# Optimization experiments

Measured on AMD Instinct MI355X. Metric: run time of the kernel, lower is better.

The kernel has to match this reference:

```python
import jax, jax.numpy as jnp
import numpy as np

H_HEADS = 8
EPS = 1e-5

def layernorm(x, g, b):
    m = jnp.mean(x, axis=-1, keepdims=True)
    v = jnp.mean(jnp.square(x - m), axis=-1, keepdims=True)
    return (x - m) * jax.lax.rsqrt(v + EPS) * g + b

def setup_inputs() -> dict:
    key = jax.random.key(0)
    ks = jax.random.split(key, 8)
    B, H, W, C = 8, 64, 64, 256
    C2 = 2 * C
    s = lambda n: 1.0 / np.sqrt(n)
    return {
        "x1": jax.random.normal(ks[0], (B, H, W, C), jnp.float32),
        "x2": jax.random.normal(ks[1], (B, H, W, C), jnp.float32),
        "norm1_g": jnp.ones((C,)), "norm1_b": jnp.zeros((C,)),
        "lin_w": jax.random.normal(ks[2], (C, C), jnp.float32) * s(C),
        "lin_b": jnp.zeros((C,)),
        "reproj_w": jax.random.normal(ks[3], (C, C), jnp.float32) * s(C),
        "reproj_b": jnp.zeros((C,)),
        "attn_norm_g": jnp.ones((C,)), "attn_norm_b": jnp.zeros((C,)),
        "norm2_g": jnp.ones((C,)), "norm2_b": jnp.zeros((C,)),
        "fc1_w": jax.random.normal(ks[4], (C2, C), jnp.float32) * s(C),
        "fc1_b": jnp.zeros((C2,)),
        "dw_w": jax.random.normal(ks[5], (C2, 1, 3, 3), jnp.float32) * s(9),
        "dw_b": jnp.zeros((C2,)),
        "ffn_n1_g": jnp.ones((C2,)), "ffn_n1_b": jnp.zeros((C2,)),
        "fc2_w": jax.random.normal(ks[6], (C, C2), jnp.float32) * s(C2),
        "fc2_b": jnp.zeros((C,)),
        "ffn_n3_g": jnp.ones((C,)), "ffn_n3_b": jnp.zeros((C,)),
    }

def reference(x1, x2, norm1_g, norm1_b, lin_w, lin_b, reproj_w, reproj_b,
              attn_norm_g, attn_norm_b, norm2_g, norm2_b, fc1_w, fc1_b,
              dw_w, dw_b, ffn_n1_g, ffn_n1_b, fc2_w, fc2_b, ffn_n3_g, ffn_n3_b):
    B, H, W, C = x1.shape
    N = H * W
    h = H_HEADS
    dk = C // h  # head key channels; value_dim == key_dim == C here
    # shared norm1 + linear projection of both streams
    n1 = layernorm(x1, norm1_g, norm1_b) @ lin_w.T + lin_b  # (B,H,W,C) queries src
    n2 = layernorm(x2, norm1_g, norm1_b) @ lin_w.T + lin_b  # (B,H,W,C) key/value src
    # (B,N,C) -> (B,h,d,N); channel dim split contiguously per head (matches torch slicing)
    q = jnp.transpose(n1.reshape(B, N, h, dk), (0, 2, 3, 1))
    k = jnp.transpose(n2.reshape(B, N, h, dk), (0, 2, 3, 1))
    v = k  # values are the same tensor slices (value_dim == key_dim)
    k = jax.nn.softmax(k, axis=-1)   # softmax over tokens N
    q = jax.nn.softmax(q, axis=2)    # softmax over head channel dim
    # linear attention: context (B,h,dk,dv), then project back to tokens
    context = jnp.einsum('bhdn,bhvn->bhdv', k, v)
    att = jnp.einsum('bhdv,bhdn->bhvn', context, q)  # (B,h,dv,N)
    agg = att.reshape(B, C, H, W)
    # 1x1 conv reprojection (value_channels -> key_channels)
    rep = jnp.einsum('bvhw,kv->bhwk', agg, reproj_w) + reproj_b  # (B,H,W,C)
    attn_out = layernorm(rep, attn_norm_g, attn_norm_b)
    # out_proj is Identity since key_dim == in_dim
    tx = attn_out + x1
    y = layernorm(tx, norm2_g, norm2_b)  # skip_ffn input
    # skip_ffn
    h1 = y @ fc1_w.T + fc1_b  # (B,H,W,2C)
    hc = jnp.transpose(h1, (0, 3, 1, 2))  # NCHW
    dw = jax.lax.conv_general_dilated(
        hc, dw_w, window_strides=(1, 1), padding='SAME',
        dimension_numbers=('NCHW', 'OIHW', 'NCHW'),
        feature_group_count=hc.shape[1])
    dw = jnp.transpose(dw + dw_b[None, :, None, None], (0, 2, 3, 1))  # NHWC
    ax = jax.nn.gelu(layernorm(dw, ffn_n1_g, ffn_n1_b), approximate=False)
    out = ax @ fc2_w.T + fc2_b
    return layernorm(out + y, ffn_n3_g, ffn_n3_b)
```

## Files before the change

### kernel.cpp

```cpp
#include <hip/hip_runtime.h>

#define BTOK 32768
#define CC 256
#define CC2 512
#define NBATCH 8

typedef __bf16 bf16x8 __attribute__((ext_vector_type(8)));
typedef float f32x4 __attribute__((ext_vector_type(4)));
typedef unsigned short u16x8 __attribute__((ext_vector_type(8)));
typedef unsigned short u16x4 __attribute__((ext_vector_type(4)));

__device__ __forceinline__ float b2f(unsigned short u) {
    return __uint_as_float(((unsigned)u) << 16);
}
__device__ __forceinline__ unsigned short f2b(float f) {
    unsigned x = __float_as_uint(f);
    return (unsigned short)((x + 0x7fffu + ((x >> 16) & 1u)) >> 16);
}
__device__ __forceinline__ float wredsum(float v) {
#pragma unroll
    for (int m = 1; m < 64; m <<= 1) v += __shfl_xor(v, m);
    return v;
}
__device__ __forceinline__ float grp4sum(float v) {
    v += __shfl_xor(v, 1);
    v += __shfl_xor(v, 2);
    return v;
}

typedef __attribute__((address_space(3))) unsigned int lds_u32;
typedef const __attribute__((address_space(1))) unsigned int glb_u32;
__device__ __forceinline__ void gload_lds16(const unsigned short* g, unsigned short* l) {
    __builtin_amdgcn_global_load_lds((glb_u32*)g, (lds_u32*)l, 16, 0, 0);
}

__global__ __launch_bounds__(256) void probe_kernel(
    const unsigned short* __restrict__ x, int* __restrict__ flag)
{
    int t = threadIdx.x;
    int c = 0;
    for (int i = t; i < 1024; i += 256) {
        unsigned e = (x[i] >> 7) & 0xFFu;
        c += (e >= 110u && e <= 135u) ? 1 : 0;
    }
#pragma unroll
    for (int m = 1; m < 64; m <<= 1) c += __shfl_xor(c, m);
    __shared__ int acc[4];
    if ((t & 63) == 0) acc[t >> 6] = c;
    __syncthreads();
    if (t == 0) *flag = ((acc[0] + acc[1] + acc[2] + acc[3]) >= 896) ? 1 : 0;
}

__global__ __launch_bounds__(256) void cvt_params_kernel(
    const int* __restrict__ flagp,
    const void* p0, const void* p1, const void* p2, const void* p3, const void* p4,
    const void* p5, const void* p6, const void* p7, const void* p8, const void* p9,
    const void* p10, const void* p11, const void* p12, const void* p13, const void* p14,
    const void* p15, const void* p16, const void* p17, const void* p18, const void* p19,
    unsigned short* __restrict__ dst)
{
    bool isb = (*flagp != 0);
    long g = (long)blockIdx.x * 256 + threadIdx.x;
    long str = (long)gridDim.x * 256;
#define CVT(src, off, n)                                                        \
    for (long i = g; i < (long)(n); i += str)                                   \
        dst[(off) + i] = isb ? ((const unsigned short*)(src))[i]                \
                             : f2b(((const float*)(src))[i]);
    CVT(p0, 0, 256)
    CVT(p1, 256, 256)
    CVT(p2, 512, 65536)
    CVT(p3, 66048, 256)
    CVT(p4, 66304, 65536)
    CVT(p5, 131840, 256)
    CVT(p6, 132096, 256)
    CVT(p7, 132352, 256)
    CVT(p8, 132608, 256)
    CVT(p9, 132864, 256)
    CVT(p10, 133120, 131072)
    CVT(p11, 264192, 512)
    for (long i = g; i < 4608; i += str) {
        int tap = (int)(i >> 9), c = (int)(i & 511);
        dst[264704 + i] = isb ? ((const unsigned short*)p12)[c * 9 + tap]
                              : f2b(((const float*)p12)[c * 9 + tap]);
    }
    CVT(p13, 269312, 512)
    CVT(p14, 269824, 512)
    CVT(p15, 270336, 512)
    CVT(p16, 270848, 131072)
    CVT(p17, 401920, 256)
    CVT(p18, 402176, 256)
    CVT(p19, 402432, 256)
#undef CVT
}

__global__ __launch_bounds__(256) void ln_dual_kernel(
    const void* __restrict__ x1, const void* __restrict__ x2,
    const unsigned short* __restrict__ g, const unsigned short* __restrict__ b,
    unsigned short* __restrict__ out, const int* __restrict__ flagp)
{
    bool isb = (*flagp != 0);
    int wid = threadIdx.x >> 6, l = threadIdx.x & 63;
    long row = (long)blockIdx.x * 4 + wid;
    const void* xsel = (row < BTOK) ? x1 : x2;
    long r = (row < BTOK) ? row : (row - BTOK);
    float f[4];
    if (isb) {
        u16x4 v = *reinterpret_cast<const u16x4*>((const unsigned short*)xsel + r * CC + l * 4);
#pragma unroll
        for (int j = 0; j < 4; j++) f[j] = b2f(v[j]);
    } else {
        f32x4 v = *reinterpret_cast<const f32x4*>((const float*)xsel + r * CC + l * 4);
#pragma unroll
        for (int j = 0; j < 4; j++) f[j] = v[j];
    }
    float mean = wredsum(f[0] + f[1] + f[2] + f[3]) * (1.f / CC);
    float d[4], sq = 0.f;
#pragma unroll
    for (int j = 0; j < 4; j++) { d[j] = f[j] - mean; sq += d[j] * d[j]; }
    float rs = rsqrtf(wredsum(sq) * (1.f / CC) + 1e-5f);
    u16x4 gv = *reinterpret_cast<const u16x4*>(g + l * 4);
    u16x4 bv = *reinterpret_cast<const u16x4*>(b + l * 4);
    u16x4 o;
#pragma unroll
    for (int j = 0; j < 4; j++) o[j] = f2b(d[j] * rs * b2f(gv[j]) + b2f(bv[j]));
    *reinterpret_cast<u16x4*>(out + row * CC + l * 4) = o;
}

template<int K>
__global__ __launch_bounds__(256) void gemm_lds_kernel(
    const unsigned short* __restrict__ A, const unsigned short* __restrict__ Wt,
    const unsigned short* __restrict__ bias, unsigned short* __restrict__ out,
    int O, int nwg)
{
    __shared__ unsigned short Asm[3][4096];
    __shared__ unsigned short Bsm[3][4096];
    int t = threadIdx.x, l = t & 63, w = t >> 6;
    int bid = blockIdx.x, cpx = nwg >> 3;
    int wg = (bid & 7) * cpx + (bid >> 3);
    int ntn = O >> 7;
    long tm = (long)(wg / ntn) << 7;
    int tn = (wg % ntn) << 7;
    int wr = (w >> 1) << 6, wc = (w & 1) << 6;

    int rloc = t >> 2;
    int q = (t & 3) ^ ((t >> 3) & 3);
    const unsigned short* ga0 = A + (tm + rloc) * K + q * 8;
    const unsigned short* ga1 = ga0 + (long)64 * K;
    const unsigned short* gb0 = Wt + (long)(tn + rloc) * K + q * 8;
    const unsigned short* gb1 = gb0 + (long)64 * K;

    int rr = l & 15;
    int sA = ((l >> 4) ^ ((rr >> 1) & 3)) << 3;
    int aoff[4], boff[4];
#pragma unroll
    for (int m = 0; m < 4; m++) aoff[m] = (wr + m * 16 + rr) * 32 + sA;
#pragma unroll
    for (int n = 0; n < 4; n++) boff[n] = (wc + n * 16 + rr) * 32 + sA;

    f32x4 acc[4][4];
#pragma unroll
    for (int m = 0; m < 4; m++)
#pragma unroll
        for (int n = 0; n < 4; n++) acc[m][n] = {0.f, 0.f, 0.f, 0.f};

    auto stage = [&](int buf, int koff) {
        gload_lds16(ga0 + koff, &Asm[buf][w * 512]);
        gload_lds16(ga1 + koff, &Asm[buf][2048 + w * 512]);
        gload_lds16(gb0 + koff, &Bsm[buf][w * 512]);
        gload_lds16(gb1 + koff, &Bsm[buf][2048 + w * 512]);
    };
    auto compute = [&](int buf) {
        bf16x8 af[4], bfr[4];
#pragma unroll
        for (int m = 0; m < 4; m++) af[m] = *reinterpret_cast<const bf16x8*>(&Asm[buf][aoff[m]]);
#pragma unroll
        for (int n = 0; n < 4; n++) bfr[n] = *reinterpret_cast<const bf16x8*>(&Bsm[buf][boff[n]]);
#pragma unroll
        for (int m = 0; m < 4; m++)
#pragma unroll
            for (int n = 0; n < 4; n++)
                acc[m][n] = __builtin_amdgcn_mfma_f32_16x16x32_bf16(af[m], bfr[n], acc[m][n], 0, 0, 0);
    };

    constexpr int NK = K / 32;
    stage(0, 0);
    stage(1, 32);
    asm volatile("s_waitcnt vmcnt(4)" ::: "memory");
    __builtin_amdgcn_s_barrier();
    asm volatile("" ::: "memory");
#pragma unroll
    for (int kt = 0; kt < NK; kt++) {
        if (kt + 2 < NK) stage((kt + 2) % 3, (kt + 2) * 32);
        compute(kt % 3);
        if (kt + 1 < NK) {
            if (kt + 2 < NK) asm volatile("s_waitcnt vmcnt(4)" ::: "memory");
            else             asm volatile("s_waitcnt vmcnt(0)" ::: "memory");
            __builtin_amdgcn_s_barrier();
            asm volatile("" ::: "memory");
        }
    }

    int orow = (l >> 4) << 2;
    int ocol = l & 15;
    float bi[4];
#pragma unroll
    for (int n = 0; n < 4; n++) bi[n] = b2f(bias[tn + wc + n * 16 + ocol]);
#pragma unroll
    for (int m = 0; m < 4; m++) {
#pragma unroll
        for (int n = 0; n < 4; n++) {
#pragma unroll
            for (int j = 0; j < 4; j++) {
                out[(tm + wr + m * 16 + orow + j) * O + tn + wc + n * 16 + ocol] =
                    f2b(acc[m][n][j] + bi[n]);
            }
        }
    }
}

#define REPS 272
template<int K, int MODE>
__global__ __launch_bounds__(512) void gemm_fused_kernel(
    const unsigned short* __restrict__ A, const unsigned short* __restrict__ Wt,
    const unsigned short* __restrict__ bias, const void* __restrict__ xin,
    const unsigned short* __restrict__ g1, const unsigned short* __restrict__ b1,
    const unsigned short* __restrict__ g2p, const unsigned short* __restrict__ b2p,
    void* __restrict__ outp, const int* __restrict__ flagp, int nwg)
{
    __shared__ unsigned short SA[3][4096];
    __shared__ unsigned short SB[3][8192];
    __shared__ unsigned short Rep[128 * REPS];
    int t = threadIdx.x, l = t & 63, w = t >> 6;
    int bid = blockIdx.x, cpx = nwg >> 3;
    int wg = (bid & 7) * cpx + (bid >> 3);
    long tm = (long)wg << 7;
    int wr = (w >> 2) << 6, wc = (w & 3) << 6;

    int rloc = t >> 2;
    int q = (t & 3) ^ ((t >> 3) & 3);
    const unsigned short* ga0 = A + (tm + rloc) * K + q * 8;
    const unsigned short* gb0 = Wt + (long)rloc * K + q * 8;
    const unsigned short* gb1 = gb0 + (long)128 * K;

    int rr = l & 15;
    int sA = ((l >> 4) ^ ((rr >> 1) & 3)) << 3;
    int aoff[4], boff[4];
#pragma unroll
    for (int m = 0; m < 4; m++) aoff[m] = (wr + m * 16 + rr) * 32 + sA;
#pragma unroll
    for (int n = 0; n < 4; n++) boff[n] = (wc + n * 16 + rr) * 32 + sA;

    f32x4 acc[4][4];
#pragma unroll
    for (int m = 0; m < 4; m++)
#pragma unroll
        for (int n = 0; n < 4; n++) acc[m][n] = {0.f, 0.f, 0.f, 0.f};

    auto stage = [&](int buf, int koff) {
        gload_lds16(ga0 + koff, &SA[buf][w * 512]);
        gload_lds16(gb0 + koff, &SB[buf][w * 512]);
        gload_lds16(gb1 + koff, &SB[buf][4096 + w * 512]);
    };
    auto compute = [&](int buf) {
        bf16x8 af[4], bfr[4];
#pragma unroll
        for (int m = 0; m < 4; m++) af[m] = *reinterpret_cast<const bf16x8*>(&SA[buf][aoff[m]]);
#pragma unroll
        for (int n = 0; n < 4; n++) bfr[n] = *reinterpret_cast<const bf16x8*>(&SB[buf][boff[n]]);
#pragma unroll
        for (int m = 0; m < 4; m++)
#pragma unroll
            for (int n = 0; n < 4; n++)
                acc[m][n] = __builtin_amdgcn_mfma_f32_16x16x32_bf16(af[m], bfr[n], acc[m][n], 0, 0, 0);
    };

    constexpr int NK = K / 32;
    stage(0, 0);
    stage(1, 32);
    asm volatile("s_waitcnt vmcnt(3)" ::: "memory");
    __builtin_amdgcn_s_barrier();
    asm volatile("" ::: "memory");
#pragma unroll
    for (int kt = 0; kt < NK; kt++) {
        if (kt + 2 < NK) stage((kt + 2) % 3, (kt + 2) * 32);
        compute(kt % 3);
        if (kt + 1 < NK) {
            if (kt + 2 < NK) asm volatile("s_waitcnt vmcnt(3)" ::: "memory");
            else             asm volatile("s_waitcnt vmcnt(0)" ::: "memory");
            __builtin_amdgcn_s_barrier();
            asm volatile("" ::: "memory");
        }
    }

    int orow = (l >> 4) << 2, ocol = l & 15;
#pragma unroll
    for (int n = 0; n < 4; n++) {
        float bi = b2f(bias[wc + n * 16 + ocol]);
#pragma unroll
        for (int m = 0; m < 4; m++)
#pragma unroll
            for (int j = 0; j < 4; j++)
                Rep[(wr + m * 16 + orow + j) * REPS + wc + n * 16 + ocol] =
                    f2b(acc[m][n][j] + bi);
    }
    __syncthreads();

    bool isb = (*flagp != 0);
    int r = t >> 2, qd = t & 3;
    long grow = tm + r;
    const unsigned short* rrow = Rep + r * REPS + qd * 8;
    u16x8 rv[8];
#pragma unroll
    for (int i = 0; i < 8; i++) rv[i] = *reinterpret_cast<const u16x8*>(rrow + i * 32);

    if constexpr (MODE == 0) {
        float s1 = 0.f;
#pragma unroll
        for (int i = 0; i < 8; i++)
#pragma unroll
            for (int j = 0; j < 8; j++) s1 += b2f(rv[i][j]);
        s1 = grp4sum(s1);
        float mean = s1 * (1.f / 256);
        float s2 = 0.f;
#pragma unroll
        for (int i = 0; i < 8; i++)
#pragma unroll
            for (int j = 0; j < 8; j++) { float d = b2f(rv[i][j]) - mean; s2 += d * d; }
        s2 = grp4sum(s2);
        float rs = rsqrtf(s2 * (1.f / 256) + 1e-5f);
        const float* xf = (const float*)xin + grow * 256 + qd * 8;
        const unsigned short* xb = (const unsigned short*)xin + grow * 256 + qd * 8;
        float tt[8][8];
        float t1 = 0.f, t2 = 0.f;
#pragma unroll
        for (int i = 0; i < 8; i++) {
            int cb = qd * 8 + i * 32;
            u16x8 gg = *reinterpret_cast<const u16x8*>(g1 + cb);
            u16x8 bb = *reinterpret_cast<const u16x8*>(b1 + cb);
            float xv[8];
            if (isb) {
                u16x8 x8 = *reinterpret_cast<const u16x8*>(xb + i * 32);
#pragma unroll
                for (int j = 0; j < 8; j++) xv[j] = b2f(x8[j]);
            } else {
                f32x4 a0 = *reinterpret_cast<const f32x4*>(xf + i * 32);
                f32x4 a1 = *reinterpret_cast<const f32x4*>(xf + i * 32 + 4);
#pragma unroll
                for (int j = 0; j < 4; j++) { xv[j] = a0[j]; xv[4 + j] = a1[j]; }
            }
#pragma unroll
            for (int j = 0; j < 8; j++) {
                float nv = (b2f(rv[i][j]) - mean) * rs * b2f(gg[j]) + b2f(bb[j]);
                float v = nv + xv[j];
                tt[i][j] = v;
                t1 += v; t2 += v * v;
            }
        }
        t1 = grp4sum(t1); t2 = grp4sum(t2);
        float mean2 = t1 * (1.f / 256);
        float rs2 = rsqrtf(t2 * (1.f / 256) - mean2 * mean2 + 1e-5f);
        unsigned short* ob = (unsigned short*)outp + grow * 256 + qd * 8;
#pragma unroll
        for (int i = 0; i < 8; i++) {
            int cb = qd * 8 + i * 32;
            u16x8 g2v = *reinterpret_cast<const u16x8*>(g2p + cb);
            u16x8 b2vv = *reinterpret_cast<const u16x8*>(b2p + cb);
            u16x8 o;
#pragma unroll
            for (int j = 0; j < 8; j++)
                o[j] = f2b((tt[i][j] - mean2) * rs2 * b2f(g2v[j]) + b2f(b2vv[j]));
            *reinterpret_cast<u16x8*>(ob + i * 32) = o;
        }
    } else {
        const unsigned short* yb = (const unsigned short*)xin + grow * 256 + qd * 8;
        u16x8 yv[8];
#pragma unroll
        for (int i = 0; i < 8; i++) yv[i] = *reinterpret_cast<const u16x8*>(yb + i * 32);
        float t1 = 0.f, t2 = 0.f;
#pragma unroll
        for (int i = 0; i < 8; i++)
#pragma unroll
            for (int j = 0; j < 8; j++) {
                float tt = b2f(rv[i][j]) + b2f(yv[i][j]);
                t1 += tt; t2 += tt * tt;
            }
        t1 = grp4sum(t1); t2 = grp4sum(t2);
        float mean2 = t1 * (1.f / 256);
        float rs2 = rsqrtf(t2 * (1.f / 256) - mean2 * mean2 + 1e-5f);
        float* of = (float*)outp + grow * 256 + qd * 8;
        unsigned short* ob = (unsigned short*)outp + grow * 256 + qd * 8;
#pragma unroll
        for (int i = 0; i < 8; i++) {
            int cb = qd * 8 + i * 32;
            u16x8 gg = *reinterpret_cast<const u16x8*>(g1 + cb);
            u16x8 bb = *reinterpret_cast<const u16x8*>(b1 + cb);
            float rvals[8];
#pragma unroll
            for (int j = 0; j < 8; j++) {
                float tt = b2f(rv[i][j]) + b2f(yv[i][j]);
                rvals[j] = (tt - mean2) * rs2 * b2f(gg[j]) + b2f(bb[j]);
            }
            if (isb) {
                u16x8 o;
#pragma unroll
                for (int j = 0; j < 8; j++) o[j] = f2b(rvals[j]);
                *reinterpret_cast<u16x8*>(ob + i * 32) = o;
            } else {
                f32x4 o0, o1;
#pragma unroll
                for (int j = 0; j < 4; j++) { o0[j] = rvals[j]; o1[j] = rvals[4 + j]; }
                *reinterpret_cast<f32x4*>(of + i * 32) = o0;
                *reinterpret_cast<f32x4*>(of + i * 32 + 4) = o1;
            }
        }
    }
}

__global__ __launch_bounds__(256) void ctx_part_kernel(
    const unsigned short* __restrict__ n2, float* __restrict__ pctx,
    float* __restrict__ pcs)
{
    int blk = blockIdx.x;
    int b = blk >> 7, hd = (blk >> 4) & 7, slab = blk & 15;
    int t = threadIdx.x;
    __shared__ float ld[32][33], eld[32][33];
    int d = t >> 3;
    int v0 = (t & 7) << 2;
    int ln_ = t >> 3;
    int lc = (t & 7) << 2;
    f32x4 acc = {0.f, 0.f, 0.f, 0.f};
    float se = 0.f;
    const unsigned short* base = n2 + ((long)b * 4096 + slab * 256) * CC + hd * 32;
    for (int n0 = 0; n0 < 256; n0 += 32) {
        u16x4 rv = *reinterpret_cast<const u16x4*>(base + (long)(n0 + ln_) * CC + lc);
#pragma unroll
        for (int j = 0; j < 4; j++) {
            float x = b2f(rv[j]);
            ld[ln_][lc + j] = x;
            eld[ln_][lc + j] = __expf(x);
        }
        __syncthreads();
#pragma unroll 4
        for (int nn = 0; nn < 32; nn++) {
            float e = eld[nn][d];
            se += e;
#pragma unroll
            for (int j = 0; j < 4; j++) acc[j] += e * ld[nn][v0 + j];
        }
        __syncthreads();
    }
    long o = ((long)slab * NBATCH * 8 + (long)b * 8 + hd) * 1024 + (long)d * 32 + v0;
#pragma unroll
    for (int j = 0; j < 4; j++) pctx[o + j] = acc[j];
    if ((t & 7) == 0)
        pcs[(long)slab * (NBATCH * 8 * 32) + ((long)(b * 8 + hd) << 5) + d] = se;
}

__global__ __launch_bounds__(256) void ctx_reduce_kernel(
    const float* __restrict__ pctx, const float* __restrict__ pcs,
    float* __restrict__ ctx)
{
    long i = (long)blockIdx.x * 256 + threadIdx.x;
    int bh = (int)(i >> 10);
    int d = (int)((i >> 5) & 31);
    float s = 0.f, ps = 0.f;
#pragma unroll
    for (int sl = 0; sl < 16; sl++) {
        s += pctx[(long)sl * 65536 + i];
        ps += pcs[(long)sl * (NBATCH * 8 * 32) + (bh << 5) + d];
    }
    ctx[i] = s / ps;
}

__global__ __launch_bounds__(256) void att_kernel(
    const unsigned short* __restrict__ n1, const float* __restrict__ ctx,
    unsigned short* __restrict__ attv)
{
    __shared__ float cl[32 * 256];
    int b = blockIdx.x >> 6, grp = blockIdx.x & 63;
    int t = threadIdx.x, wid = t >> 6, l = t & 63;
    const float* cb = ctx + (long)b * 8192;
    for (int i = 0; i < 32; i++) {
        int gidx = t + (i << 8);
        int hd_ = gidx >> 10, dd = (gidx >> 5) & 31, vv = gidx & 31;
        cl[dd * 256 + hd_ * 32 + vv] = cb[gidx];
    }
    __syncthreads();
    int base_lane = l & 56;
    long tokbase = (long)b * 4096 + grp * 64 + wid * 16;
    const f32x4* c4 = reinterpret_cast<const f32x4*>(cl);
    for (int it = 0; it < 16; it++) {
        long tok = tokbase + it;
        u16x4 rv = *reinterpret_cast<const u16x4*>(n1 + tok * CC + l * 4);
        float x[4];
#pragma unroll
        for (int j = 0; j < 4; j++) x[j] = b2f(rv[j]);
        float mx = fmaxf(fmaxf(x[0], x[1]), fmaxf(x[2], x[3]));
        mx = fmaxf(mx, __shfl_xor(mx, 1));
        mx = fmaxf(mx, __shfl_xor(mx, 2));
        mx = fmaxf(mx, __shfl_xor(mx, 4));
        float e[4], s = 0.f;
#pragma unroll
        for (int j = 0; j < 4; j++) { e[j] = __expf(x[j] - mx); s += e[j]; }
        s += __shfl_xor(s, 1);
        s += __shfl_xor(s, 2);
        s += __shfl_xor(s, 4);
        float inv = 1.f / s;
        f32x4 o = {0.f, 0.f, 0.f, 0.f};
#pragma unroll
        for (int dd = 0; dd < 32; dd++) {
            float qv = __shfl(e[dd & 3], base_lane + (dd >> 2));
            o += qv * c4[dd * 64 + l];
        }
        o *= inv;
        u16x4 ov;
#pragma unroll
        for (int j = 0; j < 4; j++) ov[j] = f2b(o[j]);
        *reinterpret_cast<u16x4*>(attv + tok * CC + l * 4) = ov;
    }
}

__global__ __launch_bounds__(256) void dw_kernel(
    const unsigned short* __restrict__ h1, const unsigned short* __restrict__ dwt,
    const unsigned short* __restrict__ dwb, const unsigned short* __restrict__ g,
    const unsigned short* __restrict__ bb, unsigned short* __restrict__ ax)
{
    int wid = threadIdx.x >> 6, l = threadIdx.x & 63;
    int pix = blockIdx.x * 4 + wid;
    int b = pix >> 12, rem = pix & 4095, py = rem >> 6, px = rem & 63;
    int c0 = l * 8;
    u16x8 wv[9];
#pragma unroll
    for (int tap = 0; tap < 9; tap++)
        wv[tap] = *reinterpret_cast<const u16x8*>(dwt + tap * CC2 + c0);
    u16x8 biasv = *reinterpret_cast<const u16x8*>(dwb + c0);
    float acc[8];
#pragma unroll
    for (int j = 0; j < 8; j++) acc[j] = b2f(biasv[j]);
#pragma unroll
    for (int ky = 0; ky < 3; ky++) {
        int ys = py + ky - 1;
        if ((unsigned)ys >= 64u) continue;
#pragma unroll
        for (int kx = 0; kx < 3; kx++) {
            int xs = px + kx - 1;
            if ((unsigned)xs >= 64u) continue;
            u16x8 pv = *reinterpret_cast<const u16x8*>(
                h1 + ((long)(b << 12) + (ys << 6) + xs) * CC2 + c0);
            int tap = ky * 3 + kx;
#pragma unroll
            for (int j = 0; j < 8; j++)
                acc[j] += b2f(pv[j]) * b2f(wv[tap][j]);
        }
    }
    float s = 0.f;
#pragma unroll
    for (int j = 0; j < 8; j++) s += acc[j];
    float mean = wredsum(s) * (1.f / CC2);
    float d[8], sq = 0.f;
#pragma unroll
    for (int j = 0; j < 8; j++) { d[j] = acc[j] - mean; sq += d[j] * d[j]; }
    float rs = rsqrtf(wredsum(sq) * (1.f / CC2) + 1e-5f);
    u16x8 gv = *reinterpret_cast<const u16x8*>(g + c0);
    u16x8 bv = *reinterpret_cast<const u16x8*>(bb + c0);
    u16x8 o;
#pragma unroll
    for (int j = 0; j < 8; j++) {
        float nv = d[j] * rs * b2f(gv[j]) + b2f(bv[j]);
        float u = 1.59576912f * nv * (1.f + 0.044715f * nv * nv);
        float gl = nv / (1.f + __expf(-u));
        o[j] = f2b(gl);
    }
    *reinterpret_cast<u16x8*>(ax + (long)pix * CC2 + c0) = o;
}

extern "C" void kernel_launch(void* const* d_in, const int* in_sizes, int n_in,
                              void* d_out, int out_size, void* d_ws, size_t ws_size,
                              hipStream_t stream)
{
    char* w = (char*)d_ws;
    const size_t S1B = (size_t)BTOK * CC * 2;
    const size_t STATSB = (size_t)(2 * NBATCH * CC + NBATCH * 8 * 32 * 32) * 4;
    const size_t PARAMS_ELEMS = 402688;
    const size_t need = 6 * S1B + STATSB + 64 + PARAMS_ELEMS * 2;
    if (ws_size < need) return;

    unsigned short* ln12 = (unsigned short*)w;
    unsigned short* n12  = (unsigned short*)(w + 2 * S1B);
    unsigned short* nn1  = n12;
    unsigned short* nn2  = n12 + (size_t)BTOK * CC;
    unsigned short* attv = ln12;
    unsigned short* ybuf = nn1;
    unsigned short* h1   = ln12;
    unsigned short* axb  = (unsigned short*)(w + 4 * S1B);
    float* pctx = (float*)(w + 4 * S1B + (2048 << 10));
    float* pcs  = (float*)(w + 4 * S1B + (2048 << 10) + (4 << 20));
    float* ctxb = (float*)(w + 6 * S1B) + 2 * NBATCH * CC;
    int*   flag = (int*)(w + 6 * S1B + STATSB);
    unsigned short* pb = (unsigned short*)(w + 6 * S1B + STATSB + 64);

    unsigned short* n1g  = pb + 0;
    unsigned short* n1b  = pb + 256;
    unsigned short* linw = pb + 512;
    unsigned short* linb = pb + 66048;
    unsigned short* repw = pb + 66304;
    unsigned short* repb = pb + 131840;
    unsigned short* ang  = pb + 132096;
    unsigned short* anb  = pb + 132352;
    unsigned short* g2   = pb + 132608;
    unsigned short* b2v  = pb + 132864;
    unsigned short* fc1w = pb + 133120;
    unsigned short* fc1b = pb + 264192;
    unsigned short* dwt  = pb + 264704;
    unsigned short* dwb  = pb + 269312;
    unsigned short* fn1g = pb + 269824;
    unsigned short* fn1b = pb + 270336;
    unsigned short* fc2w = pb + 270848;
    unsigned short* fc2b = pb + 401920;
    unsigned short* fn3g = pb + 402176;
    unsigned short* fn3b = pb + 402432;

    probe_kernel<<<1, 256, 0, stream>>>((const unsigned short*)d_in[0], flag);
    cvt_params_kernel<<<512, 256, 0, stream>>>(flag,
        d_in[2], d_in[3], d_in[4], d_in[5], d_in[6], d_in[7], d_in[8], d_in[9],
        d_in[10], d_in[11], d_in[12], d_in[13], d_in[14], d_in[15], d_in[16],
        d_in[17], d_in[18], d_in[19], d_in[20], d_in[21], pb);
    ln_dual_kernel<<<2 * BTOK / 4, 256, 0, stream>>>(d_in[0], d_in[1], n1g, n1b, ln12, flag);
    {
        int nwg = (2 * BTOK / 128) * (CC / 128);
        gemm_lds_kernel<256><<<nwg, 256, 0, stream>>>(ln12, linw, linb, n12, CC, nwg);
    }
    ctx_part_kernel<<<NBATCH * 8 * 16, 256, 0, stream>>>(nn2, pctx, pcs);
    ctx_reduce_kernel<<<256, 256, 0, stream>>>(pctx, pcs, ctxb);
    att_kernel<<<NBATCH * 64, 256, 0, stream>>>(nn1, ctxb, attv);
    {
        int nwg = BTOK / 128;
        gemm_fused_kernel<256, 0><<<nwg, 512, 0, stream>>>(
            attv, repw, repb, d_in[0], ang, anb, g2, b2v, ybuf, flag, nwg);
    }
    {
        int nwg = (BTOK / 128) * (CC2 / 128);
        gemm_lds_kernel<256><<<nwg, 256, 0, stream>>>(ybuf, fc1w, fc1b, h1, CC2, nwg);
    }
    dw_kernel<<<BTOK / 4, 256, 0, stream>>>(h1, dwt, dwb, fn1g, fn1b, axb);
    {
        int nwg = BTOK / 128;
        gemm_fused_kernel<512, 1><<<nwg, 512, 0, stream>>>(
            axb, fc2w, fc2b, ybuf, fn3g, fn3b, fn3g, fn3b, d_out, flag, nwg);
    }
}
```

Before: 196.4 us.

## Fuse norm1 layernorm into the input linear projection GEMM

Replaces the separate dual layernorm kernel and the lin projection GEMM with one kernel. Each 512-thread block normalizes 128 rows of x1/x2, using four threads per row and one-pass mean/variance, and writes them as bf16 into LDS. It then runs a 128x256 MFMA GEMM against the streamed weight, with the full K-panel of A resident in LDS. This removes the round trip of the normalized activations through global memory and one launch. In exchange it uses large LDS (64KB A plus 48KB B) and 64 registers per thread for the row values, which may lower occupancy. The one-pass variance is also slightly less numerically robust.

Result: faster. 192.5 us (-2.0%).

```diff
diff --git a/kernel.cpp b/kernel.cpp
--- a/kernel.cpp
+++ b/kernel.cpp
@@ -93,37 +93,131 @@
 #undef CVT
 }
 
-__global__ __launch_bounds__(256) void ln_dual_kernel(
+__global__ __launch_bounds__(512) void lnlin_kernel(
     const void* __restrict__ x1, const void* __restrict__ x2,
-    const unsigned short* __restrict__ g, const unsigned short* __restrict__ b,
-    unsigned short* __restrict__ out, const int* __restrict__ flagp)
-{
+    const unsigned short* __restrict__ g, const unsigned short* __restrict__ bb,
+    const unsigned short* __restrict__ Wt, const unsigned short* __restrict__ bias,
+    unsigned short* __restrict__ out, const int* __restrict__ flagp, int nwg)
+{
+    __shared__ unsigned short Alds[8 * 4096];
+    __shared__ unsigned short SB[3][8192];
+    int t = threadIdx.x, l = t & 63, w = t >> 6;
+    int bid = blockIdx.x, cpx = nwg >> 3;
+    int wg = (bid & 7) * cpx + (bid >> 3);
+    long tm = (long)wg << 7;
+    int wr = (w >> 2) << 6, wc = (w & 3) << 6;
+
+    int rloc = t >> 2;
+    int q = (t & 3) ^ ((t >> 3) & 3);
+    const unsigned short* gb0 = Wt + (long)rloc * 256 + q * 8;
+    const unsigned short* gb1 = gb0 + (long)128 * 256;
+    auto stageB = [&](int buf, int koff) {
+        gload_lds16(gb0 + koff, &SB[buf][w * 512]);
+        gload_lds16(gb1 + koff, &SB[buf][4096 + w * 512]);
+    };
+    stageB(0, 0);
+    stageB(1, 32);
+
     bool isb = (*flagp != 0);
-    int wid = threadIdx.x >> 6, l = threadIdx.x & 63;
-    long row = (long)blockIdx.x * 4 + wid;
-    const void* xsel = (row < BTOK) ? x1 : x2;
-    long r = (row < BTOK) ? row : (row - BTOK);
-    float f[4];
+    int r = t >> 2, qd = t & 3;
+    long grow = tm + r;
+    const void* xsel = (grow < BTOK) ? x1 : x2;
+    long gr = (grow < BTOK) ? grow : (grow - BTOK);
+    float xv[64];
     if (isb) {
-        u16x4 v = *reinterpret_cast<const u16x4*>((const unsigned short*)xsel + r * CC + l * 4);
-#pragma unroll
-        for (int j = 0; j < 4; j++) f[j] = b2f(v[j]);
+        const unsigned short* xb = (const unsigned short*)xsel + gr * 256 + qd * 64;
+#pragma unroll
+        for (int i = 0; i < 8; i++) {
+            u16x8 v = *reinterpret_cast<const u16x8*>(xb + i * 8);
+#pragma unroll
+            for (int j = 0; j < 8; j++) xv[i * 8 + j] = b2f(v[j]);
+        }
     } else {
-        f32x4 v = *reinterpret_cast<const f32x4*>((const float*)xsel + r * CC + l * 4);
-#pragma unroll
-        for (int j = 0; j < 4; j++) f[j] = v[j];
-    }
-    float mean = wredsum(f[0] + f[1] + f[2] + f[3]) * (1.f / CC);
-    float d[4], sq = 0.f;
-#pragma unroll
-    for (int j = 0; j < 4; j++) { d[j] = f[j] - mean; sq += d[j] * d[j]; }
-    float rs = rsqrtf(wredsum(sq) * (1.f / CC) + 1e-5f);
-    u16x4 gv = *reinterpret_cast<const u16x4*>(g + l * 4);
-    u16x4 bv = *reinterpret_cast<const u16x4*>(b + l * 4);
-    u16x4 o;
-#pragma unroll
-    for (int j = 0; j < 4; j++) o[j] = f2b(d[j] * rs * b2f(gv[j]) + b2f(bv[j]));
-    *reinterpret_cast<u16x4*>(out + row * CC + l * 4) = o;
+        const float* xf = (const float*)xsel + gr * 256 + qd * 64;
+#pragma unroll
+        for (int i = 0; i < 16; i++) {
+            f32x4 v = *reinterpret_cast<const f32x4*>(xf + i * 4);
+#pragma unroll
+            for (int j = 0; j < 4; j++) xv[i * 4 + j] = v[j];
+        }
+    }
+    float s1 = 0.f, s2 = 0.f;
+#pragma unroll
+    for (int i = 0; i < 64; i++) { s1 += xv[i]; s2 += xv[i] * xv[i]; }
+    s1 = grp4sum(s1); s2 = grp4sum(s2);
+    float mean = s1 * (1.f / 256);
+    float rs = rsqrtf(s2 * (1.f / 256) - mean * mean + 1e-5f);
+#pragma unroll
+    for (int i = 0; i < 8; i++) {
+        int c0 = qd * 64 + i * 8;
+        u16x8 gg = *reinterpret_cast<const u16x8*>(g + c0);
+        u16x8 bv = *reinterpret_cast<const u16x8*>(bb + c0);
+        u16x8 o;
+#pragma unroll
+        for (int j = 0; j < 8; j++)
+            o[j] = f2b((xv[i * 8 + j] - mean) * rs * b2f(gg[j]) + b2f(bv[j]));
+        int p = c0 >> 5;
+        int sq = (i & 3) ^ ((r >> 1) & 3);
+        *reinterpret_cast<u16x8*>(&Alds[p * 4096 + r * 32 + sq * 8]) = o;
+    }
+
+    int rr = l & 15;
+    int sA = ((l >> 4) ^ ((rr >> 1) & 3)) << 3;
+    int aoff[4], boff[4];
+#pragma unroll
+    for (int m = 0; m < 4; m++) aoff[m] = (wr + m * 16 + rr) * 32 + sA;
+#pragma unroll
+    for (int n = 0; n < 4; n++) boff[n] = (wc + n * 16 + rr) * 32 + sA;
+
+    f32x4 acc[4][4];
+#pragma unroll
+    for (int m = 0; m < 4; m++)
+#pragma unroll
+        for (int n = 0; n < 4; n++) acc[m][n] = {0.f, 0.f, 0.f, 0.f};
+
+    asm volatile("s_waitcnt vmcnt(2) lgkmcnt(0)" ::: "memory");
+    __builtin_amdgcn_s_barrier();
+    asm volatile("" ::: "memory");
+
+#pragma unroll
+    for (int kt = 0; kt < 8; kt++) {
+        if (kt + 2 < 8) stageB((kt + 2) % 3, (kt + 2) * 32);
+        bf16x8 af[4], bfr[4];
+#pragma unroll
+        for (int m = 0; m < 4; m++)
+            af[m] = *reinterpret_cast<const bf16x8*>(&Alds[kt * 4096 + aoff[m]]);
+#pragma unroll
+        for (int n = 0; n < 4; n++)
+            bfr[n] = *reinterpret_cast<const bf16x8*>(&SB[kt % 3][boff[n]]);
+#pragma unroll
+        for (int m = 0; m < 4; m++)
+#pragma unroll
+            for (int n = 0; n < 4; n++)
+                acc[m][n] = __builtin_amdgcn_mfma_f32_16x16x32_bf16(af[m], bfr[n], acc[m][n], 0, 0, 0);
+        if (kt + 1 < 8) {
+            if (kt + 2 < 8) asm volatile("s_waitcnt vmcnt(2)" ::: "memory");
+            else            asm volatile("s_waitcnt vmcnt(0)" ::: "memory");
+            __builtin_amdgcn_s_barrier();
+            asm volatile("" ::: "memory");
+        }
+    }
+
+    int orow = (l >> 4) << 2;
+    int ocol = l & 15;
+    float bi[4];
+#pragma unroll
+    for (int n = 0; n < 4; n++) bi[n] = b2f(bias[wc + n * 16 + ocol]);
+#pragma unroll
+    for (int m = 0; m < 4; m++) {
+#pragma unroll
+        for (int n = 0; n < 4; n++) {
+#pragma unroll
+            for (int j = 0; j < 4; j++) {
+                out[(tm + wr + m * 16 + orow + j) * 256 + wc + n * 16 + ocol] =
+                    f2b(acc[m][n][j] + bi[n]);
+            }
+        }
+    }
 }
 
 template<int K>
@@ -625,10 +719,10 @@
         d_in[2], d_in[3], d_in[4], d_in[5], d_in[6], d_in[7], d_in[8], d_in[9],
         d_in[10], d_in[11], d_in[12], d_in[13], d_in[14], d_in[15], d_in[16],
         d_in[17], d_in[18], d_in[19], d_in[20], d_in[21], pb);
-    ln_dual_kernel<<<2 * BTOK / 4, 256, 0, stream>>>(d_in[0], d_in[1], n1g, n1b, ln12, flag);
     {
-        int nwg = (2 * BTOK / 128) * (CC / 128);
-        gemm_lds_kernel<256><<<nwg, 256, 0, stream>>>(ln12, linw, linb, n12, CC, nwg);
+        int nwg = 2 * BTOK / 128;
+        lnlin_kernel<<<nwg, 512, 0, stream>>>(
+            d_in[0], d_in[1], n1g, n1b, linw, linb, n12, flag, nwg);
     }
     ctx_part_kernel<<<NBATCH * 8 * 16, 256, 0, stream>>>(nn2, pctx, pcs);
     ctx_reduce_kernel<<<256, 256, 0, stream>>>(pctx, pcs, ctxb);
```
